# Kernel tuning notes

Measured on AMD Instinct MI355X. Metric: run time of the kernel, lower is better.

The kernel has to match this reference:

```python
import jax, jax.numpy as jnp
import numpy as np

LEVELS = 16
N_MIN = 16
GROWTH = 1.5
TABLE_SIZE = 524288
FEAT_DIM = 2

# per-level grid resolutions (int, as in the torch buffer level_N)
LEVEL_N = [int(round(N_MIN * GROWTH ** l)) for l in range(LEVELS)]

# per-level seeds: same mixing constants as the torch code, truncated to 32-bit
# (JAX reference uses uint32 hashing to stay x64-free; hash structure is the
# standard Instant-NGP spatial hash with a per-level seed xor).
_cA = 15485907386658061715
_cB = 11400714819323198485
SEEDS = np.array([(_cA ^ (l * _cB)) & 0xFFFFFFFF for l in range(LEVELS)], dtype=np.uint32)

_P1 = np.uint32(2654435761)  # Instant-NGP prime for x
_P2 = np.uint32(805459861)   # Instant-NGP prime for y


def _fast_hash_2d(ix, iy, seed):
    # ix, iy: int32 [B, Npts]; returns int32 indices into the hash table
    h = (ix.astype(jnp.uint32) * _P1) ^ (iy.astype(jnp.uint32) * _P2) ^ seed
    return (h % jnp.uint32(TABLE_SIZE)).astype(jnp.int32)


def setup_inputs() -> dict:
    key = jax.random.key(0)
    k1, k2, k3 = jax.random.split(key, 3)
    tables = jax.random.uniform(k1, (LEVELS, TABLE_SIZE, FEAT_DIM),
                                dtype=jnp.float32, minval=-1e-4, maxval=1e-4)
    x0 = jax.random.randint(k2, (16,), 0, 3840, dtype=jnp.int32)
    y0 = jax.random.randint(k3, (16,), 0, 3840, dtype=jnp.int32)
    return {"tables": tables, "x0": x0, "y0": y0,
            "memorized_crop_size": 256, "complete_tile_size": 4096}


def reference(tables, x0, y0, memorized_crop_size, complete_tile_size):
    B = x0.shape[0]
    S = memorized_crop_size
    # pixel-center global coordinates for each crop: [B, S*S]
    xs = jnp.linspace(0.5, S - 0.5, S, dtype=jnp.float32)
    yy, xx = jnp.meshgrid(xs, xs, indexing='ij')  # ys == xs (square crop)
    pxf = (xx[None] + x0.astype(jnp.float32)[:, None, None]).reshape(B, S * S)
    pyf = (yy[None] + y0.astype(jnp.float32)[:, None, None]).reshape(B, S * S)

    feats = []
    for l in range(LEVELS):  # fixed small level loop, as in the original
        scale = jnp.float32(LEVEL_N[l] / complete_tile_size)
        gx = pxf * scale
        gy = pyf * scale
        ix0 = jnp.floor(gx).astype(jnp.int32)
        iy0 = jnp.floor(gy).astype(jnp.int32)
        ix1, iy1 = ix0 + 1, iy0 + 1
        fx = (gx - ix0.astype(jnp.float32))[..., None]  # [B, Npts, 1]
        fy = (gy - iy0.astype(jnp.float32))[..., None]
        seed = jnp.uint32(SEEDS[l])
        T = tables[l]  # [table_size, F]
        f00 = T[_fast_hash_2d(ix0, iy0, seed)]
        f10 = T[_fast_hash_2d(ix1, iy0, seed)]
        f01 = T[_fast_hash_2d(ix0, iy1, seed)]
        f11 = T[_fast_hash_2d(ix1, iy1, seed)]
        enc_l = ((1.0 - fx) * (1.0 - fy) * f00 + fx * (1.0 - fy) * f10
                 + (1.0 - fx) * fy * f01 + fx * fy * f11)
        feats.append(enc_l)

    enc = jnp.concatenate(feats, axis=-1)           # [B, Npts, L*F]
    enc = enc.reshape(B, S, S, LEVELS * FEAT_DIM)
    return jnp.transpose(enc, (0, 3, 1, 2))         # [B, L*F, S, S]
```

## Files before the change

kernel.cpp:

```cpp
#include <hip/hip_runtime.h>
#include <cstdint>
#include <cstddef>

#define LEVELS 16
#define TABLE_SIZE 524288
#define CROP 256
#define TILE 32
#define NXMAX 57

__device__ __constant__ int c_levelN[LEVELS] = {
    16, 24, 36, 54, 81, 122, 182, 273, 410, 615, 923, 1384, 2076, 3114, 4671, 7006
};
__device__ __constant__ uint32_t c_seed[LEVELS] = {
    (uint32_t)(15485907386658061715ULL ^ ( 0ULL * 11400714819323198485ULL)),
    (uint32_t)(15485907386658061715ULL ^ ( 1ULL * 11400714819323198485ULL)),
    (uint32_t)(15485907386658061715ULL ^ ( 2ULL * 11400714819323198485ULL)),
    (uint32_t)(15485907386658061715ULL ^ ( 3ULL * 11400714819323198485ULL)),
    (uint32_t)(15485907386658061715ULL ^ ( 4ULL * 11400714819323198485ULL)),
    (uint32_t)(15485907386658061715ULL ^ ( 5ULL * 11400714819323198485ULL)),
    (uint32_t)(15485907386658061715ULL ^ ( 6ULL * 11400714819323198485ULL)),
    (uint32_t)(15485907386658061715ULL ^ ( 7ULL * 11400714819323198485ULL)),
    (uint32_t)(15485907386658061715ULL ^ ( 8ULL * 11400714819323198485ULL)),
    (uint32_t)(15485907386658061715ULL ^ ( 9ULL * 11400714819323198485ULL)),
    (uint32_t)(15485907386658061715ULL ^ (10ULL * 11400714819323198485ULL)),
    (uint32_t)(15485907386658061715ULL ^ (11ULL * 11400714819323198485ULL)),
    (uint32_t)(15485907386658061715ULL ^ (12ULL * 11400714819323198485ULL)),
    (uint32_t)(15485907386658061715ULL ^ (13ULL * 11400714819323198485ULL)),
    (uint32_t)(15485907386658061715ULL ^ (14ULL * 11400714819323198485ULL)),
    (uint32_t)(15485907386658061715ULL ^ (15ULL * 11400714819323198485ULL)),
};

__global__ __launch_bounds__(256)
void HashTableEncoder2D_59339268161685_kernel(const float* __restrict__ tables,
                                              const int* __restrict__ x0,
                                              const int* __restrict__ y0,
                                              float* __restrict__ out)
{
    __shared__ float2 lds[NXMAX * NXMAX];

    const int xcd  = blockIdx.x & 7;
    const int s    = blockIdx.x >> 3;
    const int b    = 2 * xcd + (s >> 6);
    const int tile = s & 63;
    const int tx = (tile & 7) * TILE;
    const int ty = (tile >> 3) * TILE;

    const int tid = threadIdx.x;

    const float bx = (float)(x0[b] + tx) + 0.5f;
    const float by = (float)(y0[b] + ty) + 0.5f;

    float* outb = out + (size_t)b * (size_t)(32 * CROP * CROP);

    for (int l = 0; l < LEVELS; ++l) {
        const float scale = (float)c_levelN[l] * (1.0f / 4096.0f);
        const uint32_t seed = c_seed[l];

        const int ixlo = (int)floorf(bx * scale);
        const int iylo = (int)floorf(by * scale);
        const int nx = ((int)floorf((bx + 31.0f) * scale) + 1) - ixlo + 1;
        const int ny = ((int)floorf((by + 31.0f) * scale) + 1) - iylo + 1;

        __syncthreads();

        const float2* __restrict__ T =
            (const float2*)(tables + (size_t)l * (size_t)(TABLE_SIZE * 2));
        for (int c = tid; c < NXMAX * ny; c += 256) {
            const int row = c / NXMAX;
            const int col = c - row * NXMAX;
            if (col < nx) {
                const uint32_t h = ((uint32_t)(ixlo + col) * 2654435761u)
                                 ^ ((uint32_t)(iylo + row) * 805459861u) ^ seed;
                lds[c] = T[h & (TABLE_SIZE - 1)];
            }
        }
        __syncthreads();

        #pragma unroll
        for (int k = 0; k < 4; ++k) {
            const int p = tid + k * 256;
            const int j = p & (TILE - 1);
            const int i = p >> 5;
            const float gx = (bx + (float)j) * scale;
            const float gy = (by + (float)i) * scale;
            const float fxf = floorf(gx);
            const float fyf = floorf(gy);
            const float fx = gx - fxf;
            const float fy = gy - fyf;
            const int base = ((int)fyf - iylo) * NXMAX + ((int)fxf - ixlo);

            const float2 f00 = lds[base];
            const float2 f10 = lds[base + 1];
            const float2 f01 = lds[base + NXMAX];
            const float2 f11 = lds[base + NXMAX + 1];

            const float w00 = (1.0f - fx) * (1.0f - fy);
            const float w10 = fx * (1.0f - fy);
            const float w01 = (1.0f - fx) * fy;
            const float w11 = fx * fy;

            const float e0 = w00 * f00.x + w10 * f10.x + w01 * f01.x + w11 * f11.x;
            const float e1 = w00 * f00.y + w10 * f10.y + w01 * f01.y + w11 * f11.y;

            float* o = outb + (size_t)(2 * l) * (CROP * CROP)
                            + (ty + i) * CROP + (tx + j);
            __builtin_nontemporal_store(e0, o);
            __builtin_nontemporal_store(e1, o + CROP * CROP);
        }
    }
}

extern "C" void kernel_launch(void* const* d_in, const int* in_sizes, int n_in,
                              void* d_out, int out_size, void* d_ws, size_t ws_size,
                              hipStream_t stream)
{
    const float* tables = (const float*)d_in[0];
    const int*   x0     = (const int*)d_in[1];
    const int*   y0     = (const int*)d_in[2];
    float* out = (float*)d_out;

    HashTableEncoder2D_59339268161685_kernel<<<1024, 256, 0, stream>>>(tables, x0, y0, out);
}
```

Measured before the change: 60.07 us.

## Use 512 threads with two adjacent pixels per thread and vector stores

The block grows to 512 threads, and each thread now handles two horizontally adjacent pixels in one row instead of four pixels across a loop. The row-dependent interpolation terms are computed once per thread per level, and the outputs go out as 8-byte nontemporal vector stores. The LDS fill loop now strides by 512, which spreads the table gathers over more threads. The cost is more threads per block, which may limit occupancy, and the per-level barriers now synchronise a larger group.

```diff
diff --git a/kernel.cpp b/kernel.cpp
--- a/kernel.cpp
+++ b/kernel.cpp
@@ -7,6 +7,8 @@
 #define CROP 256
 #define TILE 32
 #define NXMAX 57
+
+typedef float f32x2 __attribute__((ext_vector_type(2)));
 
 __device__ __constant__ int c_levelN[LEVELS] = {
     16, 24, 36, 54, 81, 122, 182, 273, 410, 615, 923, 1384, 2076, 3114, 4671, 7006
@@ -30,7 +32,7 @@
     (uint32_t)(15485907386658061715ULL ^ (15ULL * 11400714819323198485ULL)),
 };
 
-__global__ __launch_bounds__(256)
+__global__ __launch_bounds__(512)
 void HashTableEncoder2D_59339268161685_kernel(const float* __restrict__ tables,
                                               const int* __restrict__ x0,
                                               const int* __restrict__ y0,
@@ -44,13 +46,19 @@
     const int tile = s & 63;
     const int tx = (tile & 7) * TILE;
     const int ty = (tile >> 3) * TILE;
-
     const int tid = threadIdx.x;
 
     const float bx = (float)(x0[b] + tx) + 0.5f;
     const float by = (float)(y0[b] + ty) + 0.5f;
 
-    float* outb = out + (size_t)b * (size_t)(32 * CROP * CROP);
+    const int r  = tid >> 4;
+    const int jj = (tid & 15) * 2;
+    const float pyv = by + (float)r;
+    const float px0 = bx + (float)jj;
+    const float px1 = px0 + 1.0f;
+
+    float* orow = out + (size_t)b * (size_t)(32 * CROP * CROP)
+                      + (ty + r) * CROP + (tx + jj);
 
     for (int l = 0; l < LEVELS; ++l) {
         const float scale = (float)c_levelN[l] * (1.0f / 4096.0f);
@@ -65,7 +73,7 @@
 
         const float2* __restrict__ T =
             (const float2*)(tables + (size_t)l * (size_t)(TABLE_SIZE * 2));
-        for (int c = tid; c < NXMAX * ny; c += 256) {
+        for (int c = tid; c < NXMAX * ny; c += 512) {
             const int row = c / NXMAX;
             const int col = c - row * NXMAX;
             if (col < nx) {
@@ -76,37 +84,47 @@
         }
         __syncthreads();
 
-        #pragma unroll
-        for (int k = 0; k < 4; ++k) {
-            const int p = tid + k * 256;
-            const int j = p & (TILE - 1);
-            const int i = p >> 5;
-            const float gx = (bx + (float)j) * scale;
-            const float gy = (by + (float)i) * scale;
-            const float fxf = floorf(gx);
-            const float fyf = floorf(gy);
-            const float fx = gx - fxf;
-            const float fy = gy - fyf;
-            const int base = ((int)fyf - iylo) * NXMAX + ((int)fxf - ixlo);
+        const float gy  = pyv * scale;
+        const float fyf = floorf(gy);
+        const float fy  = gy - fyf;
+        const int rowb  = ((int)fyf - iylo) * NXMAX - ixlo;
 
-            const float2 f00 = lds[base];
-            const float2 f10 = lds[base + 1];
-            const float2 f01 = lds[base + NXMAX];
-            const float2 f11 = lds[base + NXMAX + 1];
+        const float gx0 = px0 * scale;
+        const float fx0f = floorf(gx0);
+        const float fx0 = gx0 - fx0f;
+        const int base0 = rowb + (int)fx0f;
 
-            const float w00 = (1.0f - fx) * (1.0f - fy);
-            const float w10 = fx * (1.0f - fy);
-            const float w01 = (1.0f - fx) * fy;
-            const float w11 = fx * fy;
+        const float gx1 = px1 * scale;
+        const float fx1f = floorf(gx1);
+        const float fx1 = gx1 - fx1f;
+        const int base1 = rowb + (int)fx1f;
 
-            const float e0 = w00 * f00.x + w10 * f10.x + w01 * f01.x + w11 * f11.x;
-            const float e1 = w00 * f00.y + w10 * f10.y + w01 * f01.y + w11 * f11.y;
+        const float2 a00 = lds[base0];
+        const float2 a10 = lds[base0 + 1];
+        const float2 a01 = lds[base0 + NXMAX];
+        const float2 a11 = lds[base0 + NXMAX + 1];
+        const float2 b00 = lds[base1];
+        const float2 b10 = lds[base1 + 1];
+        const float2 b01 = lds[base1 + NXMAX];
+        const float2 b11 = lds[base1 + NXMAX + 1];
 
-            float* o = outb + (size_t)(2 * l) * (CROP * CROP)
-                            + (ty + i) * CROP + (tx + j);
-            __builtin_nontemporal_store(e0, o);
-            __builtin_nontemporal_store(e1, o + CROP * CROP);
-        }
+        const float ua00 = (1.0f - fx0) * (1.0f - fy);
+        const float ua10 = fx0 * (1.0f - fy);
+        const float ua01 = (1.0f - fx0) * fy;
+        const float ua11 = fx0 * fy;
+        const float ub00 = (1.0f - fx1) * (1.0f - fy);
+        const float ub10 = fx1 * (1.0f - fy);
+        const float ub01 = (1.0f - fx1) * fy;
+        const float ub11 = fx1 * fy;
+
+        f32x2 c0, c1;
+        c0.x = ua00 * a00.x + ua10 * a10.x + ua01 * a01.x + ua11 * a11.x;
+        c1.x = ua00 * a00.y + ua10 * a10.y + ua01 * a01.y + ua11 * a11.y;
+        c0.y = ub00 * b00.x + ub10 * b10.x + ub01 * b01.x + ub11 * b11.x;
+        c1.y = ub00 * b00.y + ub10 * b10.y + ub01 * b01.y + ub11 * b11.y;
+
+        __builtin_nontemporal_store(c0, (f32x2*)(orow + (size_t)(2 * l) * (CROP * CROP)));
+        __builtin_nontemporal_store(c1, (f32x2*)(orow + (size_t)(2 * l + 1) * (CROP * CROP)));
     }
 }
 
@@ -119,5 +137,5 @@
     const int*   y0     = (const int*)d_in[2];
     float* out = (float*)d_out;
 
-    HashTableEncoder2D_59339268161685_kernel<<<1024, 256, 0, stream>>>(tables, x0, y0, out);
+    HashTableEncoder2D_59339268161685_kernel<<<1024, 512, 0, stream>>>(tables, x0, y0, out);
 }
```

Measured after the change: 73.65 us. 22.6% more time.

## Gather finest level directly into registers up front, shrink LDS tile

Applied to the files above, without the earlier changes.

The finest level (15) no longer goes through the LDS staging path. Its 16 corner features per thread are gathered straight from global memory into registers at kernel start, so those gathers overlap with the LDS-staged work for levels 0-14. The LDS tile shrinks from 57x57 to 40x40 and launch bounds now request 8 blocks per SM to raise occupancy. Per-thread x-coordinate work is hoisted out of the row loop. The cost is 32 extra float registers per thread held across the whole loop, which may push register pressure against the occupancy hint.

```diff
diff --git a/kernel.cpp b/kernel.cpp
--- a/kernel.cpp
+++ b/kernel.cpp
@@ -2,41 +2,27 @@
 #include <cstdint>
 #include <cstddef>
 
-#define LEVELS 16
 #define TABLE_SIZE 524288
 #define CROP 256
 #define TILE 32
-#define NXMAX 57
+#define NXS 40
 
-__device__ __constant__ int c_levelN[LEVELS] = {
-    16, 24, 36, 54, 81, 122, 182, 273, 410, 615, 923, 1384, 2076, 3114, 4671, 7006
+__device__ __constant__ int c_levelN[15] = {
+    16, 24, 36, 54, 81, 122, 182, 273, 410, 615, 923, 1384, 2076, 3114, 4671
 };
-__device__ __constant__ uint32_t c_seed[LEVELS] = {
-    (uint32_t)(15485907386658061715ULL ^ ( 0ULL * 11400714819323198485ULL)),
-    (uint32_t)(15485907386658061715ULL ^ ( 1ULL * 11400714819323198485ULL)),
-    (uint32_t)(15485907386658061715ULL ^ ( 2ULL * 11400714819323198485ULL)),
-    (uint32_t)(15485907386658061715ULL ^ ( 3ULL * 11400714819323198485ULL)),
-    (uint32_t)(15485907386658061715ULL ^ ( 4ULL * 11400714819323198485ULL)),
-    (uint32_t)(15485907386658061715ULL ^ ( 5ULL * 11400714819323198485ULL)),
-    (uint32_t)(15485907386658061715ULL ^ ( 6ULL * 11400714819323198485ULL)),
-    (uint32_t)(15485907386658061715ULL ^ ( 7ULL * 11400714819323198485ULL)),
-    (uint32_t)(15485907386658061715ULL ^ ( 8ULL * 11400714819323198485ULL)),
-    (uint32_t)(15485907386658061715ULL ^ ( 9ULL * 11400714819323198485ULL)),
-    (uint32_t)(15485907386658061715ULL ^ (10ULL * 11400714819323198485ULL)),
-    (uint32_t)(15485907386658061715ULL ^ (11ULL * 11400714819323198485ULL)),
-    (uint32_t)(15485907386658061715ULL ^ (12ULL * 11400714819323198485ULL)),
-    (uint32_t)(15485907386658061715ULL ^ (13ULL * 11400714819323198485ULL)),
-    (uint32_t)(15485907386658061715ULL ^ (14ULL * 11400714819323198485ULL)),
-    (uint32_t)(15485907386658061715ULL ^ (15ULL * 11400714819323198485ULL)),
+#define SEED(l) ((uint32_t)(15485907386658061715ULL ^ ((uint64_t)(l) * 11400714819323198485ULL)))
+__device__ __constant__ uint32_t c_seed[15] = {
+    SEED(0),SEED(1),SEED(2),SEED(3),SEED(4),SEED(5),SEED(6),SEED(7),
+    SEED(8),SEED(9),SEED(10),SEED(11),SEED(12),SEED(13),SEED(14)
 };
 
-__global__ __launch_bounds__(256)
+__global__ __launch_bounds__(256, 8)
 void HashTableEncoder2D_59339268161685_kernel(const float* __restrict__ tables,
                                               const int* __restrict__ x0,
                                               const int* __restrict__ y0,
                                               float* __restrict__ out)
 {
-    __shared__ float2 lds[NXMAX * NXMAX];
+    __shared__ float2 lds[NXS * NXS];
 
     const int xcd  = blockIdx.x & 7;
     const int s    = blockIdx.x >> 3;
@@ -44,15 +30,41 @@
     const int tile = s & 63;
     const int tx = (tile & 7) * TILE;
     const int ty = (tile >> 3) * TILE;
-
     const int tid = threadIdx.x;
 
     const float bx = (float)(x0[b] + tx) + 0.5f;
     const float by = (float)(y0[b] + ty) + 0.5f;
 
-    float* outb = out + (size_t)b * (size_t)(32 * CROP * CROP);
+    const int j  = tid & 31;
+    const int i0 = tid >> 5;
+    const float px = bx + (float)j;
 
-    for (int l = 0; l < LEVELS; ++l) {
+    float* ocol = out + (size_t)b * (size_t)(32 * CROP * CROP)
+                      + (size_t)ty * CROP + (tx + j);
+
+    float2 g15[16];
+    {
+        const float sc = 7006.0f * (1.0f / 4096.0f);
+        const uint32_t seed = SEED(15);
+        const float gx = px * sc;
+        const int ix0 = (int)floorf(gx);
+        const uint32_t hx0 = (uint32_t)ix0 * 2654435761u;
+        const uint32_t hx1 = (uint32_t)(ix0 + 1) * 2654435761u;
+        const float2* __restrict__ T = (const float2*)tables + (size_t)15 * TABLE_SIZE;
+        #pragma unroll
+        for (int k = 0; k < 4; ++k) {
+            const float gy = (by + (float)(i0 + 8 * k)) * sc;
+            const int iy0 = (int)floorf(gy);
+            const uint32_t hy0 = ((uint32_t)iy0 * 805459861u) ^ seed;
+            const uint32_t hy1 = ((uint32_t)(iy0 + 1) * 805459861u) ^ seed;
+            g15[4 * k + 0] = T[(hx0 ^ hy0) & (TABLE_SIZE - 1)];
+            g15[4 * k + 1] = T[(hx1 ^ hy0) & (TABLE_SIZE - 1)];
+            g15[4 * k + 2] = T[(hx0 ^ hy1) & (TABLE_SIZE - 1)];
+            g15[4 * k + 3] = T[(hx1 ^ hy1) & (TABLE_SIZE - 1)];
+        }
+    }
+
+    for (int l = 0; l < 15; ++l) {
         const float scale = (float)c_levelN[l] * (1.0f / 4096.0f);
         const uint32_t seed = c_seed[l];
 
@@ -64,10 +76,10 @@
         __syncthreads();
 
         const float2* __restrict__ T =
-            (const float2*)(tables + (size_t)l * (size_t)(TABLE_SIZE * 2));
-        for (int c = tid; c < NXMAX * ny; c += 256) {
-            const int row = c / NXMAX;
-            const int col = c - row * NXMAX;
+            (const float2*)tables + (size_t)l * TABLE_SIZE;
+        for (int c = tid; c < NXS * ny; c += 256) {
+            const int row = c / NXS;
+            const int col = c - row * NXS;
             if (col < nx) {
                 const uint32_t h = ((uint32_t)(ixlo + col) * 2654435761u)
                                  ^ ((uint32_t)(iylo + row) * 805459861u) ^ seed;
@@ -76,23 +88,23 @@
         }
         __syncthreads();
 
+        const float gx = px * scale;
+        const float fxf = floorf(gx);
+        const float fx = gx - fxf;
+        const int cb = (int)fxf - ixlo;
+
         #pragma unroll
         for (int k = 0; k < 4; ++k) {
-            const int p = tid + k * 256;
-            const int j = p & (TILE - 1);
-            const int i = p >> 5;
-            const float gx = (bx + (float)j) * scale;
+            const int i = i0 + 8 * k;
             const float gy = (by + (float)i) * scale;
-            const float fxf = floorf(gx);
             const float fyf = floorf(gy);
-            const float fx = gx - fxf;
             const float fy = gy - fyf;
-            const int base = ((int)fyf - iylo) * NXMAX + ((int)fxf - ixlo);
+            const int base = ((int)fyf - iylo) * NXS + cb;
 
             const float2 f00 = lds[base];
             const float2 f10 = lds[base + 1];
-            const float2 f01 = lds[base + NXMAX];
-            const float2 f11 = lds[base + NXMAX + 1];
+            const float2 f01 = lds[base + NXS];
+            const float2 f11 = lds[base + NXS + 1];
 
             const float w00 = (1.0f - fx) * (1.0f - fy);
             const float w10 = fx * (1.0f - fy);
@@ -102,10 +114,41 @@
             const float e0 = w00 * f00.x + w10 * f10.x + w01 * f01.x + w11 * f11.x;
             const float e1 = w00 * f00.y + w10 * f10.y + w01 * f01.y + w11 * f11.y;
 
-            float* o = outb + (size_t)(2 * l) * (CROP * CROP)
-                            + (ty + i) * CROP + (tx + j);
-            __builtin_nontemporal_store(e0, o);
-            __builtin_nontemporal_store(e1, o + CROP * CROP);
+            float* o = ocol + i * CROP;
+            __builtin_nontemporal_store(e0, o + (size_t)(2 * l)     * (CROP * CROP));
+            __builtin_nontemporal_store(e1, o + (size_t)(2 * l + 1) * (CROP * CROP));
+        }
+    }
+
+    {
+        const float sc = 7006.0f * (1.0f / 4096.0f);
+        const float gx = px * sc;
+        const float fxf = floorf(gx);
+        const float fx = gx - fxf;
+
+        #pragma unroll
+        for (int k = 0; k < 4; ++k) {
+            const int i = i0 + 8 * k;
+            const float gy = (by + (float)i) * sc;
+            const float fyf = floorf(gy);
+            const float fy = gy - fyf;
+
+            const float w00 = (1.0f - fx) * (1.0f - fy);
+            const float w10 = fx * (1.0f - fy);
+            const float w01 = (1.0f - fx) * fy;
+            const float w11 = fx * fy;
+
+            const float2 f00 = g15[4 * k + 0];
+            const float2 f10 = g15[4 * k + 1];
+            const float2 f01 = g15[4 * k + 2];
+            const float2 f11 = g15[4 * k + 3];
+
+            const float e0 = w00 * f00.x + w10 * f10.x + w01 * f01.x + w11 * f11.x;
+            const float e1 = w00 * f00.y + w10 * f10.y + w01 * f01.y + w11 * f11.y;
+
+            float* o = ocol + i * CROP;
+            __builtin_nontemporal_store(e0, o + (size_t)30 * (CROP * CROP));
+            __builtin_nontemporal_store(e1, o + (size_t)31 * (CROP * CROP));
         }
     }
 }
```

Measured after the change: 69.65 us. 1.16x slower.

## Batch-gather small levels with one barrier and vectorize per-thread outputs

Applied to the files above, without the earlier changes.

The first 12 levels have small, compile-time-sized grid footprints. They are now gathered together into a dedicated LDS region, along with level 12's gather, before a single barrier, replacing two barriers per level. Each thread now computes 4 adjacent pixels in a row and writes them with 128-bit nontemporal stores, and the y-interpolation terms are hoisted out of the pixel loop. This exposes more concurrent global gathers and cuts synchronization, at the cost of hardcoded per-level footprint sizes that must cover every input offset.

```diff
diff --git a/kernel.cpp b/kernel.cpp
--- a/kernel.cpp
+++ b/kernel.cpp
@@ -2,33 +2,27 @@
 #include <cstdint>
 #include <cstddef>
 
-#define LEVELS 16
 #define TABLE_SIZE 524288
 #define CROP 256
 #define TILE 32
-#define NXMAX 57
+#define NXS 57
 
-__device__ __constant__ int c_levelN[LEVELS] = {
+typedef float f32x4 __attribute__((ext_vector_type(4)));
+
+__device__ __constant__ int c_levelN[16] = {
     16, 24, 36, 54, 81, 122, 182, 273, 410, 615, 923, 1384, 2076, 3114, 4671, 7006
 };
-__device__ __constant__ uint32_t c_seed[LEVELS] = {
-    (uint32_t)(15485907386658061715ULL ^ ( 0ULL * 11400714819323198485ULL)),
-    (uint32_t)(15485907386658061715ULL ^ ( 1ULL * 11400714819323198485ULL)),
-    (uint32_t)(15485907386658061715ULL ^ ( 2ULL * 11400714819323198485ULL)),
-    (uint32_t)(15485907386658061715ULL ^ ( 3ULL * 11400714819323198485ULL)),
-    (uint32_t)(15485907386658061715ULL ^ ( 4ULL * 11400714819323198485ULL)),
-    (uint32_t)(15485907386658061715ULL ^ ( 5ULL * 11400714819323198485ULL)),
-    (uint32_t)(15485907386658061715ULL ^ ( 6ULL * 11400714819323198485ULL)),
-    (uint32_t)(15485907386658061715ULL ^ ( 7ULL * 11400714819323198485ULL)),
-    (uint32_t)(15485907386658061715ULL ^ ( 8ULL * 11400714819323198485ULL)),
-    (uint32_t)(15485907386658061715ULL ^ ( 9ULL * 11400714819323198485ULL)),
-    (uint32_t)(15485907386658061715ULL ^ (10ULL * 11400714819323198485ULL)),
-    (uint32_t)(15485907386658061715ULL ^ (11ULL * 11400714819323198485ULL)),
-    (uint32_t)(15485907386658061715ULL ^ (12ULL * 11400714819323198485ULL)),
-    (uint32_t)(15485907386658061715ULL ^ (13ULL * 11400714819323198485ULL)),
-    (uint32_t)(15485907386658061715ULL ^ (14ULL * 11400714819323198485ULL)),
-    (uint32_t)(15485907386658061715ULL ^ (15ULL * 11400714819323198485ULL)),
+#define SEED(l) ((uint32_t)(15485907386658061715ULL ^ ((uint64_t)(l) * 11400714819323198485ULL)))
+__device__ __constant__ uint32_t c_seed[16] = {
+    SEED(0),SEED(1),SEED(2),SEED(3),SEED(4),SEED(5),SEED(6),SEED(7),
+    SEED(8),SEED(9),SEED(10),SEED(11),SEED(12),SEED(13),SEED(14),SEED(15)
 };
+
+constexpr int SN[12]   = {16,24,36,54,81,122,182,273,410,615,923,1384};
+constexpr int SNX[12]  = {4,4,4,4,4,4,5,6,7,8,10,14};
+constexpr int SOFF[12] = {0,16,32,48,64,80,96,121,157,206,270,370};
+constexpr uint32_t SSEED[12] = {SEED(0),SEED(1),SEED(2),SEED(3),SEED(4),SEED(5),
+                                SEED(6),SEED(7),SEED(8),SEED(9),SEED(10),SEED(11)};
 
 __global__ __launch_bounds__(256)
 void HashTableEncoder2D_59339268161685_kernel(const float* __restrict__ tables,
@@ -36,7 +30,8 @@
                                               const int* __restrict__ y0,
                                               float* __restrict__ out)
 {
-    __shared__ float2 lds[NXMAX * NXMAX];
+    __shared__ float2 ldsS[566];
+    __shared__ float2 ldsB[NXS * NXS];
 
     const int xcd  = blockIdx.x & 7;
     const int s    = blockIdx.x >> 3;
@@ -44,69 +39,125 @@
     const int tile = s & 63;
     const int tx = (tile & 7) * TILE;
     const int ty = (tile >> 3) * TILE;
-
     const int tid = threadIdx.x;
 
     const float bx = (float)(x0[b] + tx) + 0.5f;
     const float by = (float)(y0[b] + ty) + 0.5f;
 
-    float* outb = out + (size_t)b * (size_t)(32 * CROP * CROP);
+    const int j0 = (tid & 7) * 4;
+    const int i  = tid >> 3;
+    const float py  = by + (float)i;
+    const float px0 = bx + (float)j0;
 
-    for (int l = 0; l < LEVELS; ++l) {
-        const float scale = (float)c_levelN[l] * (1.0f / 4096.0f);
+    float* obase = out + (size_t)b * (size_t)(32 * CROP * CROP)
+                       + (size_t)(ty + i) * CROP + (tx + j0);
+
+    auto stage_big = [&](int l) {
+        const float sc = (float)c_levelN[l] * (1.0f / 4096.0f);
         const uint32_t seed = c_seed[l];
-
-        const int ixlo = (int)floorf(bx * scale);
-        const int iylo = (int)floorf(by * scale);
-        const int nx = ((int)floorf((bx + 31.0f) * scale) + 1) - ixlo + 1;
-        const int ny = ((int)floorf((by + 31.0f) * scale) + 1) - iylo + 1;
-
-        __syncthreads();
-
-        const float2* __restrict__ T =
-            (const float2*)(tables + (size_t)l * (size_t)(TABLE_SIZE * 2));
-        for (int c = tid; c < NXMAX * ny; c += 256) {
-            const int row = c / NXMAX;
-            const int col = c - row * NXMAX;
+        const int ixlo = (int)floorf(bx * sc);
+        const int iylo = (int)floorf(by * sc);
+        const int nx = ((int)floorf((bx + 31.0f) * sc) + 1) - ixlo + 1;
+        const int ny = ((int)floorf((by + 31.0f) * sc) + 1) - iylo + 1;
+        const float2* __restrict__ T = (const float2*)tables + (size_t)l * TABLE_SIZE;
+        const int tot = NXS * ny;
+        for (int c = tid; c < tot; c += 256) {
+            const int row = c / NXS;
+            const int col = c - row * NXS;
             if (col < nx) {
                 const uint32_t h = ((uint32_t)(ixlo + col) * 2654435761u)
                                  ^ ((uint32_t)(iylo + row) * 805459861u) ^ seed;
-                lds[c] = T[h & (TABLE_SIZE - 1)];
+                ldsB[c] = T[h & (TABLE_SIZE - 1)];
             }
         }
-        __syncthreads();
+    };
 
+    auto compute_big = [&](int l) {
+        const float sc = (float)c_levelN[l] * (1.0f / 4096.0f);
+        const int ixlo = (int)floorf(bx * sc);
+        const int iylo = (int)floorf(by * sc);
+        const float gy  = py * sc;
+        const float fyf = floorf(gy);
+        const float fy  = gy - fyf;
+        const int rowb  = ((int)fyf - iylo) * NXS - ixlo;
+        f32x4 e0, e1;
         #pragma unroll
-        for (int k = 0; k < 4; ++k) {
-            const int p = tid + k * 256;
-            const int j = p & (TILE - 1);
-            const int i = p >> 5;
-            const float gx = (bx + (float)j) * scale;
-            const float gy = (by + (float)i) * scale;
+        for (int t = 0; t < 4; ++t) {
+            const float gx  = (px0 + (float)t) * sc;
             const float fxf = floorf(gx);
-            const float fyf = floorf(gy);
-            const float fx = gx - fxf;
-            const float fy = gy - fyf;
-            const int base = ((int)fyf - iylo) * NXMAX + ((int)fxf - ixlo);
-
-            const float2 f00 = lds[base];
-            const float2 f10 = lds[base + 1];
-            const float2 f01 = lds[base + NXMAX];
-            const float2 f11 = lds[base + NXMAX + 1];
-
+            const float fx  = gx - fxf;
+            const int base  = rowb + (int)fxf;
+            const float2 f00 = ldsB[base];
+            const float2 f10 = ldsB[base + 1];
+            const float2 f01 = ldsB[base + NXS];
+            const float2 f11 = ldsB[base + NXS + 1];
             const float w00 = (1.0f - fx) * (1.0f - fy);
             const float w10 = fx * (1.0f - fy);
             const float w01 = (1.0f - fx) * fy;
             const float w11 = fx * fy;
+            e0[t] = w00 * f00.x + w10 * f10.x + w01 * f01.x + w11 * f11.x;
+            e1[t] = w00 * f00.y + w10 * f10.y + w01 * f01.y + w11 * f11.y;
+        }
+        __builtin_nontemporal_store(e0, (f32x4*)(obase + (size_t)(2 * l)     * (CROP * CROP)));
+        __builtin_nontemporal_store(e1, (f32x4*)(obase + (size_t)(2 * l + 1) * (CROP * CROP)));
+    };
 
-            const float e0 = w00 * f00.x + w10 * f10.x + w01 * f01.x + w11 * f11.x;
-            const float e1 = w00 * f00.y + w10 * f10.y + w01 * f01.y + w11 * f11.y;
+    #pragma unroll
+    for (int l = 0; l < 12; ++l) {
+        const int NX = SNX[l], CNT = NX * NX, OFF = SOFF[l];
+        if (tid < CNT) {
+            const float sc = (float)SN[l] * (1.0f / 4096.0f);
+            const int ixlo = (int)floorf(bx * sc);
+            const int iylo = (int)floorf(by * sc);
+            const int row = tid / NX;
+            const int col = tid - row * NX;
+            const uint32_t h = ((uint32_t)(ixlo + col) * 2654435761u)
+                             ^ ((uint32_t)(iylo + row) * 805459861u) ^ SSEED[l];
+            ldsS[OFF + tid] =
+                ((const float2*)tables)[(size_t)l * TABLE_SIZE + (h & (TABLE_SIZE - 1))];
+        }
+    }
+    stage_big(12);
+    __syncthreads();
 
-            float* o = outb + (size_t)(2 * l) * (CROP * CROP)
-                            + (ty + i) * CROP + (tx + j);
-            __builtin_nontemporal_store(e0, o);
-            __builtin_nontemporal_store(e1, o + CROP * CROP);
+    #pragma unroll
+    for (int l = 0; l < 12; ++l) {
+        const int NX = SNX[l], OFF = SOFF[l];
+        const float sc = (float)SN[l] * (1.0f / 4096.0f);
+        const int ixlo = (int)floorf(bx * sc);
+        const int iylo = (int)floorf(by * sc);
+        const float gy  = py * sc;
+        const float fyf = floorf(gy);
+        const float fy  = gy - fyf;
+        const int rowb  = OFF + ((int)fyf - iylo) * NX - ixlo;
+        f32x4 e0, e1;
+        #pragma unroll
+        for (int t = 0; t < 4; ++t) {
+            const float gx  = (px0 + (float)t) * sc;
+            const float fxf = floorf(gx);
+            const float fx  = gx - fxf;
+            const int base  = rowb + (int)fxf;
+            const float2 f00 = ldsS[base];
+            const float2 f10 = ldsS[base + 1];
+            const float2 f01 = ldsS[base + NX];
+            const float2 f11 = ldsS[base + NX + 1];
+            const float w00 = (1.0f - fx) * (1.0f - fy);
+            const float w10 = fx * (1.0f - fy);
+            const float w01 = (1.0f - fx) * fy;
+            const float w11 = fx * fy;
+            e0[t] = w00 * f00.x + w10 * f10.x + w01 * f01.x + w11 * f11.x;
+            e1[t] = w00 * f00.y + w10 * f10.y + w01 * f01.y + w11 * f11.y;
         }
+        __builtin_nontemporal_store(e0, (f32x4*)(obase + (size_t)(2 * l)     * (CROP * CROP)));
+        __builtin_nontemporal_store(e1, (f32x4*)(obase + (size_t)(2 * l + 1) * (CROP * CROP)));
+    }
+    compute_big(12);
+
+    for (int l = 13; l < 16; ++l) {
+        __syncthreads();
+        stage_big(l);
+        __syncthreads();
+        compute_big(l);
     }
 }
 
```

Measured after the change: 69.74 us. +16.1%, slower.
